# Kernel tuning notes

Hardware: AMD Instinct MI355X
Metric: run time of the kernel (lower is better)

The kernel has to match this reference:

```python
import jax, jax.numpy as jnp
import numpy as np

B, C, H, W = 16, 512, 32, 32
NH, HD = 8, 64
CTX_DIM, L = 768, 512
EPS = 1e-5


def setup_inputs() -> dict:
    key = jax.random.key(0)
    ks = jax.random.split(key, 10)
    x = jax.random.normal(ks[0], (B, C, H, W), dtype=jnp.float32)
    context = jax.random.normal(ks[1], (B, L, CTX_DIM), dtype=jnp.float32)
    context_mask = jax.random.randint(ks[2], (B, L), 0, 2).astype(bool)
    context_mask = context_mask.at[:, 0].set(True)  # guarantee >=1 valid key per row
    s = 0.02
    ln_w = jnp.ones((C,), jnp.float32)
    ln_b = jnp.zeros((C,), jnp.float32)
    Wq = jax.random.normal(ks[3], (C, C), jnp.float32) * s
    Wk = jax.random.normal(ks[4], (C, C), jnp.float32) * s
    Wv = jax.random.normal(ks[5], (C, C), jnp.float32) * s
    Wo = jax.random.normal(ks[6], (C, C), jnp.float32) * s
    Wctx = jax.random.normal(ks[7], (C, CTX_DIM), jnp.float32) * s
    return {"x": x, "context": context, "context_mask": context_mask,
            "ln_w": ln_w, "ln_b": ln_b, "Wq": Wq, "Wk": Wk, "Wv": Wv,
            "Wo": Wo, "Wctx": Wctx}


def _layernorm(x, w, b):
    mu = jnp.mean(x, axis=-1, keepdims=True)
    var = jnp.mean(jnp.square(x - mu), axis=-1, keepdims=True)
    return (x - mu) * jax.lax.rsqrt(var + EPS) * w + b


def reference(x, context, context_mask, ln_w, ln_b, Wq, Wk, Wv, Wo, Wctx):
    b, c, h, w = x.shape
    n = h * w
    hidden = x.reshape(b, c, n).transpose(0, 2, 1)          # [b, n, c]
    hidden_norm = _layernorm(hidden, ln_w, ln_b)
    ctx = jnp.einsum('bld,cd->blc', context, Wctx)          # context_proj

    q = jnp.einsum('bnc,ec->bne', hidden_norm, Wq).reshape(b, n, NH, HD).transpose(0, 2, 1, 3)
    k = jnp.einsum('blc,ec->ble', ctx, Wk).reshape(b, -1, NH, HD).transpose(0, 2, 1, 3)
    v = jnp.einsum('blc,ec->ble', ctx, Wv).reshape(b, -1, NH, HD).transpose(0, 2, 1, 3)

    scale = HD ** -0.5
    scores = jnp.einsum('bhnd,bhld->bhnl', q, k) * scale    # [b,H,n,L]
    mask4 = context_mask[:, None, None, :]                  # [b,1,1,L]
    scores = jnp.where(mask4, scores, -jnp.inf)
    all_invalid = ~jnp.any(mask4, axis=-1, keepdims=True)   # [b,1,1,1]
    scores = jnp.where(all_invalid, 0.0, scores)
    attn = jax.nn.softmax(scores, axis=-1)
    attn = jnp.where(mask4, attn, 0.0)
    attn = jnp.where(all_invalid, 0.0, attn)

    out = jnp.einsum('bhnl,bhld->bhnd', attn, v)            # [b,H,n,hd]
    out = out.transpose(0, 2, 1, 3).reshape(b, n, c)
    out = jnp.einsum('bnc,ec->bne', out, Wo)
    out = out + hidden
    return out.transpose(0, 2, 1).reshape(b, c, h, w)
```

## Files before the change

kernel.cpp:

```cpp
#include <hip/hip_runtime.h>

#define B_   16
#define C_   512
#define N_   1024
#define L_   512
#define CTX_ 768
#define NH_  8
#define HD_  64
#define EPS_ 1e-5f

typedef short bfrag  __attribute__((ext_vector_type(8)));
typedef short bfrag4 __attribute__((ext_vector_type(4)));
typedef float f32x4  __attribute__((ext_vector_type(4)));

__device__ __forceinline__ ushort f2bf(float f) {
  union { float f; unsigned u; } v; v.f = f;
  unsigned r = v.u + 0x7fffu + ((v.u >> 16) & 1u);
  return (ushort)(r >> 16);
}

__device__ __forceinline__ f32x4 mfma16(bfrag a, bfrag b, f32x4 c) {
  return __builtin_amdgcn_mfma_f32_16x16x32_bf16(a, b, c, 0, 0, 0);
}
__device__ __forceinline__ f32x4 mfma16k16(bfrag4 a, bfrag4 b, f32x4 c) {
  return __builtin_amdgcn_mfma_f32_16x16x16bf16_1k(a, b, c, 0, 0, 0);
}
__device__ __forceinline__ unsigned cvt_pk_bf16(float lo, float hi) {
  unsigned d;
  asm("v_cvt_pk_bf16_f32 %0, %1, %2" : "=v"(d) : "v"(lo), "v"(hi));
  return d;
}

__device__ __forceinline__ void g2l16(const ushort* g, ushort* l) {
  __builtin_amdgcn_global_load_lds(
      (const __attribute__((address_space(1))) void*)g,
      (__attribute__((address_space(3))) void*)l, 16, 0, 0);
}

__global__ __launch_bounds__(256) void cast5_kernel(
    const float* __restrict__ s0, const float* __restrict__ s1,
    const float* __restrict__ s2, const float* __restrict__ s3,
    const float* __restrict__ s4,
    ushort* __restrict__ d0, ushort* __restrict__ d1, ushort* __restrict__ d2,
    ushort* __restrict__ d3, ushort* __restrict__ d4) {
  int i = blockIdx.x * 256 + threadIdx.x;
  const float* src; ushort* dst; int off;
  if      (i < 98304)  { src = s0; dst = d0; off = i; }
  else if (i < 163840) { src = s1; dst = d1; off = i - 98304; }
  else if (i < 229376) { src = s2; dst = d2; off = i - 163840; }
  else if (i < 294912) { src = s3; dst = d3; off = i - 229376; }
  else                 { src = s4; dst = d4; off = i - 294912; }
  float4 vv = ((const float4*)src)[off];
  ushort4 o;
  o.x = f2bf(vv.x); o.y = f2bf(vv.y); o.z = f2bf(vv.z); o.w = f2bf(vv.w);
  ((ushort4*)dst)[off] = o;
}

__global__ __launch_bounds__(1024) void ln_stats(const float* __restrict__ x,
                                                 float* __restrict__ mu_out,
                                                 float* __restrict__ rs_out) {
  const int b  = blockIdx.x;
  const int n0 = blockIdx.y * 64;
  const int tid = threadIdx.x;
  const int nx = tid & 63, cg = tid >> 6;
  const float* xb = x + (size_t)b * C_ * N_;

  float s = 0.f, s2 = 0.f;
  for (int c = cg; c < C_; c += 16) {
    float v = xb[(size_t)c * N_ + n0 + nx];
    s += v; s2 += v * v;
  }
  __shared__ float red[2][16][64];
  red[0][cg][nx] = s; red[1][cg][nx] = s2;
  __syncthreads();
  if (cg == 0) {
    float ss = 0.f, ss2 = 0.f;
#pragma unroll
    for (int i = 0; i < 16; ++i) { ss += red[0][i][nx]; ss2 += red[1][i][nx]; }
    float m  = ss * (1.f / C_);
    float var = ss2 * (1.f / C_) - m * m;
    mu_out[(size_t)b * N_ + n0 + nx] = m;
    rs_out[(size_t)b * N_ + n0 + nx] = rsqrtf(var + EPS_);
  }
}

__device__ __forceinline__ void gemm_core(const ushort* __restrict__ A,
                                          const ushort* __restrict__ W,
                                          int K, ushort* la, ushort* lb,
                                          f32x4 acc[4][4],
                                          int tid, int wm, int we, int col, int rg) {
  const int lane = tid & 63, w = tid >> 6;
  const int rloc = lane >> 2, pt = lane & 3;
  const int pts = pt ^ ((rloc >> 1) & 3);
  const int qsel = (rg ^ ((col >> 1) & 3)) * 8;

  for (int k0 = 0; k0 < K; k0 += 32) {
#pragma unroll
    for (int c = 0; c < 2; ++c) {
      const int chunk = w + c * 4;
      const int row = chunk * 16 + rloc;
      g2l16(A + (size_t)row * K + k0 + pts * 8, la + chunk * 512);
      g2l16(W + (size_t)row * K + k0 + pts * 8, lb + chunk * 512);
    }
    __syncthreads();
    bfrag af[4], bf[4];
#pragma unroll
    for (int i = 0; i < 4; ++i) {
      af[i] = *(const bfrag*)&la[(wm + i * 16 + col) * 32 + qsel];
      bf[i] = *(const bfrag*)&lb[(we + i * 16 + col) * 32 + qsel];
    }
#pragma unroll
    for (int i = 0; i < 4; ++i)
#pragma unroll
      for (int j = 0; j < 4; ++j)
        acc[i][j] = mfma16(af[i], bf[j], acc[i][j]);
    __syncthreads();
  }
}

__global__ __launch_bounds__(256) void gemm_kv(const ushort* __restrict__ A,
                                               const ushort* __restrict__ Wk,
                                               const ushort* __restrict__ Wv,
                                               ushort* __restrict__ Ko,
                                               ushort* __restrict__ Vo) {
  __shared__ ushort la[128 * 32];
  __shared__ ushort lb[128 * 32];
  const int isv = blockIdx.y >> 2;
  const ushort* W = isv ? Wv : Wk;
  ushort* out = isv ? Vo : Ko;
  const int m0 = blockIdx.x * 128, e0 = (blockIdx.y & 3) * 128;
  const int tid = threadIdx.x, lane = tid & 63, w = tid >> 6;
  const int wm = (w >> 1) * 64, we = (w & 1) * 64;
  const int col = lane & 15, rg = lane >> 4;

  f32x4 acc[4][4] = {};
  gemm_core(A + (size_t)m0 * C_, W + (size_t)e0 * C_, C_, la, lb, acc, tid, wm, we, col, rg);

#pragma unroll
  for (int i = 0; i < 4; ++i)
#pragma unroll
    for (int j = 0; j < 4; ++j)
#pragma unroll
      for (int r = 0; r < 4; ++r)
        out[(size_t)(m0 + wm + i * 16 + rg * 4 + r) * 512 + e0 + we + j * 16 + col] =
            f2bf(acc[i][j][r]);
}

__global__ __launch_bounds__(256) void gemm_res(const ushort* __restrict__ A,
                                                const ushort* __restrict__ W,
                                                const float* __restrict__ x,
                                                float* __restrict__ out) {
  __shared__ ushort la[128 * 32];
  __shared__ ushort lb[128 * 32];
  __shared__ float T[16][132];
  const int m0 = blockIdx.x * 128, e0 = blockIdx.y * 128;
  const int tid = threadIdx.x, lane = tid & 63, w = tid >> 6;
  const int wm = (w >> 1) * 64, we = (w & 1) * 64;
  const int col = lane & 15, rg = lane >> 4;

  f32x4 acc[4][4] = {};
  gemm_core(A + (size_t)m0 * C_, W + (size_t)e0 * C_, C_, la, lb, acc, tid, wm, we, col, rg);

  const int b = m0 >> 10, n0l = m0 & 1023;
#pragma unroll
  for (int g = 0; g < 8; ++g) {
    if ((w & 1) == (g >> 2)) {
      const int j = g & 3;
#pragma unroll
      for (int i = 0; i < 4; ++i)
        *(f32x4*)&T[col][wm + i * 16 + rg * 4] = acc[i][j];
    }
    __syncthreads();
    const int n = tid & 127;
    for (int cc = tid >> 7; cc < 16; cc += 2) {
      const int c = e0 + g * 16 + cc;
      const size_t idx = (size_t)b * C_ * N_ + (size_t)c * N_ + n0l + n;
      out[idx] = T[cc][n] + x[idx];
    }
    __syncthreads();
  }
}

__global__ __launch_bounds__(256) void gemm_ctx(const float* __restrict__ Ap,
                                                const ushort* __restrict__ W,
                                                ushort* __restrict__ outp) {
  __shared__ ushort la[128 * 40];
  __shared__ ushort lb[128 * 40];
  const int m0 = blockIdx.x * 128, e0 = blockIdx.y * 128;
  const int tid = threadIdx.x, lane = tid & 63, w = tid >> 6;
  const int wm = (w >> 1) * 64, we = (w & 1) * 64;
  const int col = lane & 15, rg = lane >> 4;
  const int srow = tid >> 1, sh = (tid & 1) * 16;
  const int K = CTX_;

  f32x4 acc[4][4] = {};

  for (int k0 = 0; k0 < K; k0 += 32) {
    {
      const float* ap = &Ap[(size_t)(m0 + srow) * K + k0 + sh];
      float4 f0 = ((const float4*)ap)[0];
      float4 f1 = ((const float4*)ap)[1];
      float4 f2 = ((const float4*)ap)[2];
      float4 f3 = ((const float4*)ap)[3];
      union { int4 v; ushort u[8]; } p0, p1;
      p0.u[0] = f2bf(f0.x); p0.u[1] = f2bf(f0.y); p0.u[2] = f2bf(f0.z); p0.u[3] = f2bf(f0.w);
      p0.u[4] = f2bf(f1.x); p0.u[5] = f2bf(f1.y); p0.u[6] = f2bf(f1.z); p0.u[7] = f2bf(f1.w);
      p1.u[0] = f2bf(f2.x); p1.u[1] = f2bf(f2.y); p1.u[2] = f2bf(f2.z); p1.u[3] = f2bf(f2.w);
      p1.u[4] = f2bf(f3.x); p1.u[5] = f2bf(f3.y); p1.u[6] = f2bf(f3.z); p1.u[7] = f2bf(f3.w);
      *(int4*)&la[srow * 40 + sh]     = p0.v;
      *(int4*)&la[srow * 40 + sh + 8] = p1.v;
      const ushort* wp = &W[(size_t)(e0 + srow) * K + k0 + sh];
      *(int4*)&lb[srow * 40 + sh]     = *(const int4*)wp;
      *(int4*)&lb[srow * 40 + sh + 8] = *(const int4*)(wp + 8);
    }
    __syncthreads();
    bfrag af[4], bf[4];
#pragma unroll
    for (int i = 0; i < 4; ++i) {
      af[i] = *(const bfrag*)&la[(wm + i * 16 + col) * 40 + rg * 8];
      bf[i] = *(const bfrag*)&lb[(we + i * 16 + col) * 40 + rg * 8];
    }
#pragma unroll
    for (int i = 0; i < 4; ++i)
#pragma unroll
      for (int j = 0; j < 4; ++j)
        acc[i][j] = mfma16(af[i], bf[j], acc[i][j]);
    __syncthreads();
  }

#pragma unroll
  for (int i = 0; i < 4; ++i)
#pragma unroll
    for (int j = 0; j < 4; ++j)
#pragma unroll
      for (int r = 0; r < 4; ++r)
        outp[(size_t)(m0 + wm + i * 16 + rg * 4 + r) * 512 + e0 + we + j * 16 + col] =
            f2bf(acc[i][j][r]);
}

__global__ __launch_bounds__(256) void gemm_lnq(const float* __restrict__ x,
                                                const float* __restrict__ mu,
                                                const float* __restrict__ rs,
                                                const float* __restrict__ lnw,
                                                const float* __restrict__ lnb,
                                                const ushort* __restrict__ W,
                                                ushort* __restrict__ out) {
  __shared__ ushort la[128 * 40];
  __shared__ ushort lb[128 * 40];
  const int m0 = blockIdx.x * 128, e0 = blockIdx.y * 128;
  const int b = m0 >> 10, n0l = m0 & 1023;
  const int tid = threadIdx.x, lane = tid & 63, w = tid >> 6;
  const int wm = (w >> 1) * 64, we = (w & 1) * 64;
  const int col = lane & 15, rg = lane >> 4;
  const int nloc = tid & 127, chalf = (tid >> 7) * 16;
  const int srow = tid >> 1, sh = (tid & 1) * 16;

  const float muv = mu[(size_t)b * N_ + n0l + nloc];
  const float rsv = rs[(size_t)b * N_ + n0l + nloc];
  const float nmr = -muv * rsv;
  const float* xb = x + (size_t)b * C_ * N_ + n0l + nloc;

  f32x4 acc[4][4] = {};

  for (int k0 = 0; k0 < C_; k0 += 32) {
    {
      union { int4 v[2]; ushort u[16]; } pk;
#pragma unroll
      for (int i = 0; i < 16; ++i) {
        const int c = k0 + chalf + i;
        const float xv = xb[(size_t)c * N_];
        const float t = fmaf(xv, rsv, nmr);
        pk.u[i] = f2bf(fmaf(t, lnw[c], lnb[c]));
      }
      *(int4*)&la[nloc * 40 + chalf]     = pk.v[0];
      *(int4*)&la[nloc * 40 + chalf + 8] = pk.v[1];
      const ushort* wp = &W[(size_t)(e0 + srow) * C_ + k0 + sh];
      *(int4*)&lb[srow * 40 + sh]     = *(const int4*)wp;
      *(int4*)&lb[srow * 40 + sh + 8] = *(const int4*)(wp + 8);
    }
    __syncthreads();
    bfrag af[4], bf[4];
#pragma unroll
    for (int i = 0; i < 4; ++i) {
      af[i] = *(const bfrag*)&la[(wm + i * 16 + col) * 40 + rg * 8];
      bf[i] = *(const bfrag*)&lb[(we + i * 16 + col) * 40 + rg * 8];
    }
#pragma unroll
    for (int i = 0; i < 4; ++i)
#pragma unroll
      for (int j = 0; j < 4; ++j)
        acc[i][j] = mfma16(af[i], bf[j], acc[i][j]);
    __syncthreads();
  }

#pragma unroll
  for (int i = 0; i < 4; ++i)
#pragma unroll
    for (int j = 0; j < 4; ++j)
#pragma unroll
      for (int r = 0; r < 4; ++r)
        out[(size_t)(m0 + wm + i * 16 + rg * 4 + r) * 512 + e0 + we + j * 16 + col] =
            f2bf(acc[i][j][r]);
}

__global__ __launch_bounds__(256) void attn_mfma(const ushort* __restrict__ q,
                                                 const ushort* __restrict__ k,
                                                 const ushort* __restrict__ v,
                                                 const int* __restrict__ mask,
                                                 ushort* __restrict__ o) {
  __shared__ ushort Kl[64 * 72];
  __shared__ ushort Vt[64 * 72];
  __shared__ float mlb[64];

  const int h = blockIdx.y, b = blockIdx.z;
  const int q0 = blockIdx.x * 128;
  const int tid = threadIdx.x, lane = tid & 63, w = tid >> 6;
  const int col = lane & 15, rg = lane >> 4;
  const int wq = w * 32;
  const float C1 = 0.18033688011112042f;

  bfrag qf[2][2];
#pragma unroll
  for (int mi = 0; mi < 2; ++mi)
#pragma unroll
    for (int kc = 0; kc < 2; ++kc)
      qf[mi][kc] = *(const bfrag*)
          &q[((size_t)b * N_ + q0 + wq + mi * 16 + col) * C_ + h * HD_ + kc * 32 + rg * 8];

  f32x4 oa[2][4] = {};
  float l_part[2] = {0.f, 0.f};

  for (int l0 = 0; l0 < L_; l0 += 64) {
#pragma unroll
    for (int it = 0; it < 2; ++it) {
      const int idx = it * 256 + tid;
      const int key = idx >> 3, part = idx & 7;
      *(int4*)&Kl[key * 72 + part * 8] =
          *(const int4*)&k[((size_t)b * L_ + l0 + key) * C_ + h * HD_ + part * 8];
    }
#pragma unroll
    for (int it = 0; it < 4; ++it) {
      const int idx = it * 256 + tid;
      const int key = idx & 63, d0 = (idx >> 6) * 4;
      ushort4 vv = *(const ushort4*)&v[((size_t)b * L_ + l0 + key) * C_ + h * HD_ + d0];
      Vt[(d0 + 0) * 72 + key] = vv.x;
      Vt[(d0 + 1) * 72 + key] = vv.y;
      Vt[(d0 + 2) * 72 + key] = vv.z;
      Vt[(d0 + 3) * 72 + key] = vv.w;
    }
    if (tid < 64) mlb[tid] = mask[b * L_ + l0 + tid] ? 0.f : -1e30f;
    __syncthreads();

    f32x4 s2[2][4] = {};
#pragma unroll
    for (int kc = 0; kc < 2; ++kc) {
      bfrag kf[4];
#pragma unroll
      for (int ni = 0; ni < 4; ++ni)
        kf[ni] = *(const bfrag*)&Kl[(ni * 16 + col) * 72 + kc * 32 + rg * 8];
#pragma unroll
      for (int mi = 0; mi < 2; ++mi)
#pragma unroll
        for (int ni = 0; ni < 4; ++ni)
          s2[mi][ni] = mfma16(kf[ni], qf[mi][kc], s2[mi][ni]);
    }
    bfrag4 pf[2][4];
#pragma unroll
    for (int ni = 0; ni < 4; ++ni) {
      const f32x4 bias4 = *(const f32x4*)&mlb[ni * 16 + rg * 4];
#pragma unroll
      for (int mi = 0; mi < 2; ++mi) {
        const float p0 = exp2f(fmaf(s2[mi][ni][0], C1, bias4[0]));
        const float p1 = exp2f(fmaf(s2[mi][ni][1], C1, bias4[1]));
        const float p2 = exp2f(fmaf(s2[mi][ni][2], C1, bias4[2]));
        const float p3 = exp2f(fmaf(s2[mi][ni][3], C1, bias4[3]));
        l_part[mi] += (p0 + p1) + (p2 + p3);
        union { bfrag4 v; unsigned u[2]; } pk;
        pk.u[0] = cvt_pk_bf16(p0, p1);
        pk.u[1] = cvt_pk_bf16(p2, p3);
        pf[mi][ni] = pk.v;
      }
    }
#pragma unroll
    for (int ni = 0; ni < 4; ++ni) {
      bfrag4 vf[4];
#pragma unroll
      for (int di = 0; di < 4; ++di)
        vf[di] = *(const bfrag4*)&Vt[(di * 16 + col) * 72 + ni * 16 + rg * 4];
#pragma unroll
      for (int mi = 0; mi < 2; ++mi)
#pragma unroll
        for (int di = 0; di < 4; ++di)
          oa[mi][di] = mfma16k16(pf[mi][ni], vf[di], oa[mi][di]);
    }
    __syncthreads();
  }

  float linv[2][4];
#pragma unroll
  for (int mi = 0; mi < 2; ++mi) {
    float l = l_part[mi];
    l += __shfl_xor(l, 16);
    l += __shfl_xor(l, 32);
#pragma unroll
    for (int r = 0; r < 4; ++r) {
      int lv = __builtin_amdgcn_ds_bpermute((rg * 4 + r) * 4, __float_as_int(l));
      linv[mi][r] = 1.f / __int_as_float(lv);
    }
  }
#pragma unroll
  for (int mi = 0; mi < 2; ++mi)
#pragma unroll
    for (int r = 0; r < 4; ++r) {
      const size_t row = (size_t)b * N_ + q0 + wq + mi * 16 + rg * 4 + r;
#pragma unroll
      for (int di = 0; di < 4; ++di)
        o[row * C_ + h * HD_ + di * 16 + col] = f2bf(oa[mi][di][r] * linv[mi][r]);
    }
}

extern "C" void kernel_launch(void* const* d_in, const int* in_sizes, int n_in,
                              void* d_out, int out_size, void* d_ws, size_t ws_size,
                              hipStream_t stream) {
  (void)in_sizes; (void)n_in; (void)out_size; (void)ws_size;
  const float* x       = (const float*)d_in[0];
  const float* context = (const float*)d_in[1];
  const int*   mask    = (const int*)d_in[2];
  const float* ln_w    = (const float*)d_in[3];
  const float* ln_b    = (const float*)d_in[4];
  const float* Wq      = (const float*)d_in[5];
  const float* Wk      = (const float*)d_in[6];
  const float* Wv      = (const float*)d_in[7];
  const float* Wo      = (const float*)d_in[8];
  const float* Wctx    = (const float*)d_in[9];

  char* wsb = (char*)d_ws;
  ushort* qb    = (ushort*)(wsb + 0);
  ushort* kb    = (ushort*)(wsb + 16777216);
  ushort* vb    = (ushort*)(wsb + 25165824);
  ushort* atto  = (ushort*)(wsb + 33554432);
  ushort* ctx   = (ushort*)(wsb + 50331648);
  ushort* wctxb = (ushort*)(wsb + 58720256);
  ushort* wqb   = (ushort*)(wsb + 59506688);
  ushort* wkb   = (ushort*)(wsb + 60030976);
  ushort* wvb   = (ushort*)(wsb + 60555264);
  ushort* wob   = (ushort*)(wsb + 61079552);
  float*  mub   = (float*)(wsb + 61603840);
  float*  rsb   = (float*)(wsb + 61669376);

  cast5_kernel<<<1408, 256, 0, stream>>>(Wctx, Wq, Wk, Wv, Wo,
                                         wctxb, wqb, wkb, wvb, wob);
  ln_stats<<<dim3(B_, N_ / 64), 1024, 0, stream>>>(x, mub, rsb);
  gemm_ctx<<<dim3(64, 4), 256, 0, stream>>>(context, wctxb, ctx);
  gemm_kv<<<dim3(64, 8), 256, 0, stream>>>(ctx, wkb, wvb, kb, vb);
  gemm_lnq<<<dim3(128, 4), 256, 0, stream>>>(x, mub, rsb, ln_w, ln_b, wqb, qb);
  attn_mfma<<<dim3(N_ / 128, NH_, B_), 256, 0, stream>>>(qb, kb, vb, mask, atto);
  gemm_res<<<dim3(128, 4), 256, 0, stream>>>(atto, wob, x, (float*)d_out);
}
```

Before: 170.8 us.

## Double-buffer K/V tiles in attention kernel with register prefetch

Converts the attention kernel's K, V and mask shared-memory tiles into two buffers. The next tile's global loads go into registers before the current tile's MFMA work and are written to the other buffer afterwards, which also drops one barrier per iteration. This is meant to hide global load latency behind compute, at the cost of double the LDS footprint and extra registers that may reduce occupancy.

```diff
diff --git a/kernel.cpp b/kernel.cpp
--- a/kernel.cpp
+++ b/kernel.cpp
@@ -308,9 +308,9 @@
                                                  const ushort* __restrict__ v,
                                                  const int* __restrict__ mask,
                                                  ushort* __restrict__ o) {
-  __shared__ ushort Kl[64 * 72];
-  __shared__ ushort Vt[64 * 72];
-  __shared__ float mlb[64];
+  __shared__ ushort Kl[2][64 * 72];
+  __shared__ ushort Vt[2][64 * 72];
+  __shared__ float mlb[2][64];
 
   const int h = blockIdx.y, b = blockIdx.z;
   const int q0 = blockIdx.x * 128;
@@ -330,34 +330,59 @@
   f32x4 oa[2][4] = {};
   float l_part[2] = {0.f, 0.f};
 
-  for (int l0 = 0; l0 < L_; l0 += 64) {
+  {
 #pragma unroll
     for (int it = 0; it < 2; ++it) {
       const int idx = it * 256 + tid;
       const int key = idx >> 3, part = idx & 7;
-      *(int4*)&Kl[key * 72 + part * 8] =
-          *(const int4*)&k[((size_t)b * L_ + l0 + key) * C_ + h * HD_ + part * 8];
+      *(int4*)&Kl[0][key * 72 + part * 8] =
+          *(const int4*)&k[((size_t)b * L_ + key) * C_ + h * HD_ + part * 8];
     }
 #pragma unroll
     for (int it = 0; it < 4; ++it) {
       const int idx = it * 256 + tid;
       const int key = idx & 63, d0 = (idx >> 6) * 4;
-      ushort4 vv = *(const ushort4*)&v[((size_t)b * L_ + l0 + key) * C_ + h * HD_ + d0];
-      Vt[(d0 + 0) * 72 + key] = vv.x;
-      Vt[(d0 + 1) * 72 + key] = vv.y;
-      Vt[(d0 + 2) * 72 + key] = vv.z;
-      Vt[(d0 + 3) * 72 + key] = vv.w;
-    }
-    if (tid < 64) mlb[tid] = mask[b * L_ + l0 + tid] ? 0.f : -1e30f;
-    __syncthreads();
-
+      ushort4 vv = *(const ushort4*)&v[((size_t)b * L_ + key) * C_ + h * HD_ + d0];
+      Vt[0][(d0 + 0) * 72 + key] = vv.x;
+      Vt[0][(d0 + 1) * 72 + key] = vv.y;
+      Vt[0][(d0 + 2) * 72 + key] = vv.z;
+      Vt[0][(d0 + 3) * 72 + key] = vv.w;
+    }
+    if (tid < 64) mlb[0][tid] = mask[b * L_ + tid] ? 0.f : -1e30f;
+  }
+  __syncthreads();
+
+  for (int t = 0; t < 8; ++t) {
+    const int cur = t & 1;
+    int4 kreg[2];
+    ushort4 vreg[4];
+    float mreg = 0.f;
+    if (t < 7) {
+      const int l0n = (t + 1) * 64;
+#pragma unroll
+      for (int it = 0; it < 2; ++it) {
+        const int idx = it * 256 + tid;
+        const int key = idx >> 3, part = idx & 7;
+        kreg[it] = *(const int4*)&k[((size_t)b * L_ + l0n + key) * C_ + h * HD_ + part * 8];
+      }
+#pragma unroll
+      for (int it = 0; it < 4; ++it) {
+        const int idx = it * 256 + tid;
+        const int key = idx & 63, d0 = (idx >> 6) * 4;
+        vreg[it] = *(const ushort4*)&v[((size_t)b * L_ + l0n + key) * C_ + h * HD_ + d0];
+      }
+      if (tid < 64) mreg = mask[b * L_ + l0n + tid] ? 0.f : -1e30f;
+    }
+
+    const ushort* Kc = &Kl[cur][0];
+    const ushort* Vc = &Vt[cur][0];
     f32x4 s2[2][4] = {};
 #pragma unroll
     for (int kc = 0; kc < 2; ++kc) {
       bfrag kf[4];
 #pragma unroll
       for (int ni = 0; ni < 4; ++ni)
-        kf[ni] = *(const bfrag*)&Kl[(ni * 16 + col) * 72 + kc * 32 + rg * 8];
+        kf[ni] = *(const bfrag*)&Kc[(ni * 16 + col) * 72 + kc * 32 + rg * 8];
 #pragma unroll
       for (int mi = 0; mi < 2; ++mi)
 #pragma unroll
@@ -367,7 +392,7 @@
     bfrag4 pf[2][4];
 #pragma unroll
     for (int ni = 0; ni < 4; ++ni) {
-      const f32x4 bias4 = *(const f32x4*)&mlb[ni * 16 + rg * 4];
+      const f32x4 bias4 = *(const f32x4*)&mlb[cur][ni * 16 + rg * 4];
 #pragma unroll
       for (int mi = 0; mi < 2; ++mi) {
         const float p0 = exp2f(fmaf(s2[mi][ni][0], C1, bias4[0]));
@@ -386,12 +411,32 @@
       bfrag4 vf[4];
 #pragma unroll
       for (int di = 0; di < 4; ++di)
-        vf[di] = *(const bfrag4*)&Vt[(di * 16 + col) * 72 + ni * 16 + rg * 4];
+        vf[di] = *(const bfrag4*)&Vc[(di * 16 + col) * 72 + ni * 16 + rg * 4];
 #pragma unroll
       for (int mi = 0; mi < 2; ++mi)
 #pragma unroll
         for (int di = 0; di < 4; ++di)
           oa[mi][di] = mfma16k16(pf[mi][ni], vf[di], oa[mi][di]);
+    }
+
+    if (t < 7) {
+      const int nb = cur ^ 1;
+#pragma unroll
+      for (int it = 0; it < 2; ++it) {
+        const int idx = it * 256 + tid;
+        const int key = idx >> 3, part = idx & 7;
+        *(int4*)&Kl[nb][key * 72 + part * 8] = kreg[it];
+      }
+#pragma unroll
+      for (int it = 0; it < 4; ++it) {
+        const int idx = it * 256 + tid;
+        const int key = idx & 63, d0 = (idx >> 6) * 4;
+        Vt[nb][(d0 + 0) * 72 + key] = vreg[it].x;
+        Vt[nb][(d0 + 1) * 72 + key] = vreg[it].y;
+        Vt[nb][(d0 + 2) * 72 + key] = vreg[it].z;
+        Vt[nb][(d0 + 3) * 72 + key] = vreg[it].w;
+      }
+      if (tid < 64) mlb[nb][tid] = mreg;
     }
     __syncthreads();
   }
```

Result: faster. 167.0 us (-2.2%).
